# Performance work log

Measured on AMD Instinct MI355X. Metric: run time of the kernel, lower is better.

## Reference

```python
import jax, jax.numpy as jnp
import numpy as np

D_MODEL = 1024
NHEAD = 16
HEAD_DIM = D_MODEL // NHEAD
MAX_LEN = 4096
ROPE_BASE = 500.0


def _rope_tables(L, dim):
    inv_freq = 1.0 / (ROPE_BASE ** (jnp.arange(0, dim, 2, dtype=jnp.float32) / dim))
    t = jnp.arange(L, dtype=jnp.float32)
    freqs = jnp.einsum('i,j->ij', t, inv_freq)  # [L, dim/2]
    emb = jnp.concatenate([freqs, freqs], axis=-1)  # [L, dim]
    return jnp.cos(emb), jnp.sin(emb)


def _rotate_half(x):
    x1, x2 = jnp.split(x, 2, axis=-1)
    return jnp.concatenate([-x2, x1], axis=-1)


def _apply_rope(x, cos, sin):
    return x * cos + _rotate_half(x) * sin


def setup_inputs() -> dict:
    key = jax.random.key(0)
    ks = jax.random.split(key, 6)
    B, L = 4, 2048
    bound_qkv = 1.0 / np.sqrt(D_MODEL)
    x = jax.random.normal(ks[0], (B, L, D_MODEL), dtype=jnp.float32)
    key_padding_mask = jnp.zeros((B, L), dtype=bool)
    W_qkv = jax.random.uniform(ks[1], (3 * D_MODEL, D_MODEL), jnp.float32, -bound_qkv, bound_qkv)
    b_qkv = jax.random.uniform(ks[2], (3 * D_MODEL,), jnp.float32, -bound_qkv, bound_qkv)
    W_out = jax.random.uniform(ks[3], (D_MODEL, D_MODEL), jnp.float32, -bound_qkv, bound_qkv)
    b_out = jax.random.uniform(ks[4], (D_MODEL,), jnp.float32, -bound_qkv, bound_qkv)
    return {"x": x, "key_padding_mask": key_padding_mask,
            "W_qkv": W_qkv, "b_qkv": b_qkv, "W_out": W_out, "b_out": b_out}


def reference(x, key_padding_mask, W_qkv, b_qkv, W_out, b_out):
    B, L, D = x.shape
    H, hd = NHEAD, HEAD_DIM
    qkv = x @ W_qkv.T + b_qkv  # [B, L, 3D]
    q, k, v = jnp.split(qkv, 3, axis=-1)
    # [B, H, L, hd]
    q = q.reshape(B, L, H, hd).transpose(0, 2, 1, 3)
    k = k.reshape(B, L, H, hd).transpose(0, 2, 1, 3)
    v = v.reshape(B, L, H, hd).transpose(0, 2, 1, 3)
    cos, sin = _rope_tables(L, hd)  # [L, hd]
    q = _apply_rope(q, cos, sin)
    k = _apply_rope(k, cos, sin)
    scores = jnp.einsum('bhqd,bhkd->bhqk', q, k) / jnp.sqrt(jnp.float32(hd))
    mask = key_padding_mask[:, None, None, :]  # [B,1,1,L]
    scores = jnp.where(mask, -jnp.inf, scores)
    attn = jax.nn.softmax(scores, axis=-1)
    out = jnp.einsum('bhqk,bhkd->bhqd', attn, v)
    out = out.transpose(0, 2, 1, 3).reshape(B, L, D)
    return out @ W_out.T + b_out
```

## Files before the change

kernel.cpp:

```cpp
#include <hip/hip_runtime.h>
#include <stdint.h>

typedef __attribute__((ext_vector_type(8))) __bf16 bf16x8;
typedef __attribute__((ext_vector_type(4))) short short4v;
typedef __attribute__((ext_vector_type(4))) float f32x4;

#if __has_builtin(__builtin_amdgcn_exp2f)
#define EXP2(x) __builtin_amdgcn_exp2f(x)
#else
#define EXP2(x) exp2f(x)
#endif

__device__ __forceinline__ short f2bf(float f) {
  union { float f; uint32_t u; } v; v.f = f;
  uint32_t r = (v.u + 0x7fffu + ((v.u >> 16) & 1u)) >> 16;
  return (short)(uint16_t)r;
}

__device__ __forceinline__ uint32_t pk2bf(float a, float b) {
  union { __bf16 h; uint16_t u; } x, y;
  x.h = (__bf16)a; y.h = (__bf16)b;
  return (uint32_t)x.u | ((uint32_t)y.u << 16);
}

__device__ __forceinline__ void gl2lds16(const void* g, const void* lds) {
  __builtin_amdgcn_global_load_lds(
      (const __attribute__((address_space(1))) void*)(uintptr_t)g,
      (__attribute__((address_space(3))) void*)(uint32_t)(uintptr_t)lds,
      16, 0, 0);
}

__device__ __forceinline__ bf16x8 frag8(const short* p) {
  return *(const bf16x8*)(const void*)p;
}

__global__ void convert3_k(const float* __restrict__ s0, short* __restrict__ d0, int n0,
                           const float* __restrict__ s1, short* __restrict__ d1, int n1,
                           const float* __restrict__ s2, short* __restrict__ d2, int n2) {
  int i = blockIdx.x * blockDim.x + threadIdx.x;
  int t0 = n0 >> 2, t1 = t0 + (n1 >> 2), t2 = t1 + (n2 >> 2);
  const float* s; short* d; int off;
  if (i < t0) { s = s0; d = d0; off = i; }
  else if (i < t1) { s = s1; d = d1; off = i - t0; }
  else if (i < t2) { s = s2; d = d2; off = i - t1; }
  else return;
  float4 v = ((const float4*)s)[off];
  short4v o;
  o.x = f2bf(v.x); o.y = f2bf(v.y); o.z = f2bf(v.z); o.w = f2bf(v.w);
  *(short4v*)(d + off * 4) = o;
}

__global__ void rope_tab_k(float* __restrict__ cosT, float* __restrict__ sinT,
                           const unsigned char* __restrict__ mask, float* __restrict__ maskf) {
  int i = blockIdx.x * blockDim.x + threadIdx.x;
  int pos = i >> 5, j = i & 31;
  float invf = exp2f(-(float)j * (8.965784284662087f / 32.0f));
  float ang = (float)pos * invf;
  float s, c;
  sincosf(ang, &s, &c);
  cosT[i] = c; sinT[i] = s;
  if (i < 8192) maskf[i] = mask[i] ? -1e30f : 0.0f;
}

template <int EPI>
__global__ __launch_bounds__(256, 3)
void gemm_bt_k(const short* __restrict__ A, const short* __restrict__ Bm,
               const float* __restrict__ bias, int N, int K,
               float* __restrict__ Cout,
               const float* __restrict__ cosT, const float* __restrict__ sinT,
               short* __restrict__ Qb, short* __restrict__ Kb, short* __restrict__ Vt) {
  __shared__ short As[2][128 * 32];
  __shared__ short Bs[2][128 * 32];
  const int tid = threadIdx.x;
  const int lane = tid & 63;
  const int w = tid >> 6;
  const int g = lane >> 4, l15 = lane & 15;
  const int wm = (w >> 1) * 64, wn = (w & 1) * 64;
  const int bm = blockIdx.x, bn = blockIdx.y;

  const int rseg = lane >> 2;
  const int cofs = ((lane & 3) ^ ((lane >> 3) & 3)) * 8;
  const int sA0 = w, sA1 = w + 4;
  const int arow0 = (bm * 128 + sA0 * 16 + rseg) * K;
  const int arow1 = (bm * 128 + sA1 * 16 + rseg) * K;
  const int brow0 = (bn * 128 + sA0 * 16 + rseg) * K;
  const int brow1 = (bn * 128 + sA1 * 16 + rseg) * K;

  const int rsw = (l15 >> 1) & 3;

  f32x4 acc[4][4];
#pragma unroll
  for (int i = 0; i < 4; i++)
#pragma unroll
    for (int j = 0; j < 4; j++) acc[i][j] = f32x4{0.f, 0.f, 0.f, 0.f};

  gl2lds16(A + arow0 + cofs, &As[0][sA0 * 512]);
  gl2lds16(A + arow1 + cofs, &As[0][sA1 * 512]);
  gl2lds16(Bm + brow0 + cofs, &Bs[0][sA0 * 512]);
  gl2lds16(Bm + brow1 + cofs, &Bs[0][sA1 * 512]);

  int cur = 0;
  for (int k0 = 0; k0 < K; k0 += 32, cur ^= 1) {
    __syncthreads();
    int nxt = cur ^ 1;
    int k1 = k0 + 32;
    if (k1 < K) {
      gl2lds16(A + arow0 + k1 + cofs, &As[nxt][sA0 * 512]);
      gl2lds16(A + arow1 + k1 + cofs, &As[nxt][sA1 * 512]);
      gl2lds16(Bm + brow0 + k1 + cofs, &Bs[nxt][sA0 * 512]);
      gl2lds16(Bm + brow1 + k1 + cofs, &Bs[nxt][sA1 * 512]);
    }
    bf16x8 af[4], bf[4];
#pragma unroll
    for (int im = 0; im < 4; im++) af[im] = frag8(&As[cur][(wm + im * 16 + l15) * 32 + (g ^ rsw) * 8]);
#pragma unroll
    for (int jn = 0; jn < 4; jn++) bf[jn] = frag8(&Bs[cur][(wn + jn * 16 + l15) * 32 + (g ^ rsw) * 8]);
#pragma unroll
    for (int im = 0; im < 4; im++)
#pragma unroll
      for (int jn = 0; jn < 4; jn++)
        acc[im][jn] = __builtin_amdgcn_mfma_f32_16x16x32_bf16(af[im], bf[jn], acc[im][jn], 0, 0, 0);
  }

  const int row0 = bm * 128 + wm + g * 4;
  const int col0 = bn * 128 + wn;

  if (EPI == 0) {
#pragma unroll
    for (int jn = 0; jn < 4; jn++) {
      float bb = bias[col0 + jn * 16 + l15];
#pragma unroll
      for (int im = 0; im < 4; im++)
#pragma unroll
        for (int r = 0; r < 4; r++) {
          int row = row0 + im * 16 + r;
          Cout[row * N + col0 + jn * 16 + l15] = acc[im][jn][r] + bb;
        }
    }
  } else {
#pragma unroll
    for (int jn = 0; jn < 4; jn++) {
      float bb = bias[col0 + jn * 16 + l15];
#pragma unroll
      for (int im = 0; im < 4; im++)
#pragma unroll
        for (int r = 0; r < 4; r++) acc[im][jn][r] += bb;
    }
    const int sector = col0 >> 10;
    const int h = (col0 & 1023) >> 6;
    if (sector == 2) {
#pragma unroll
      for (int jn = 0; jn < 4; jn++) {
        int d = jn * 16 + l15;
#pragma unroll
        for (int im = 0; im < 4; im++) {
          int row = row0 + im * 16;
          int b = row >> 11, pos = row & 2047;
          union { uint32_t u[2]; short4v s4; } pw;
          pw.u[0] = pk2bf(acc[im][jn][0], acc[im][jn][1]);
          pw.u[1] = pk2bf(acc[im][jn][2], acc[im][jn][3]);
          *(short4v*)&Vt[((b * 16 + h) * 64 + d) * 2048 + pos] = pw.s4;
        }
      }
    } else {
      short* dst = (sector == 0) ? Qb : Kb;
      const float scl = (sector == 0) ? 0.18033688011112042f : 1.0f;
#pragma unroll
      for (int jn = 0; jn < 4; jn++) {
        int d = jn * 16 + l15;
        int j = d & 31;
#pragma unroll
        for (int im = 0; im < 4; im++)
#pragma unroll
          for (int r = 0; r < 4; r++) {
            int row = row0 + im * 16 + r;
            int b = row >> 11, pos = row & 2047;
            float c = cosT[pos * 32 + j];
            float s = sinT[pos * 32 + j];
            float xv = acc[im][jn][r];
            float xp = acc[im][jn ^ 2][r];
            float rot = (jn < 2) ? -xp : xp;
            dst[((b * 16 + h) * 2048 + pos) * 64 + d] = f2bf((xv * c + rot * s) * scl);
          }
      }
    }
  }
}

__global__ __launch_bounds__(128, 4)
void attn_k(const short* __restrict__ Qb, const short* __restrict__ Kb,
            const short* __restrict__ Vt, const float* __restrict__ maskf,
            short* __restrict__ attn) {
  __shared__ short Ks[2][32 * 64];
  __shared__ short Vs[2][64 * 32];
  __shared__ short Ps[2][32 * 32];
  const int tid = threadIdx.x, lane = tid & 63, w = tid >> 6;
  const int g = lane >> 4, l15 = lane & 15;
  const int swk = l15 & 7;
  const int fv = (l15 ^ (l15 >> 2)) & 3;
  const int qt = blockIdx.x, bh = blockIdx.y;
  const int b = bh >> 4, h = bh & 15;

  bf16x8 aq[2][2];
#pragma unroll
  for (int qi = 0; qi < 2; qi++)
#pragma unroll
    for (int kc = 0; kc < 2; kc++) {
      int q = qt * 64 + w * 32 + qi * 16 + l15;
      aq[qi][kc] = *(const bf16x8*)(const void*)(Qb + (bh * 2048 + q) * 64 + kc * 32 + g * 8);
    }
  bf16x8 aone;
#pragma unroll
  for (int i = 0; i < 8; i++) aone[i] = (__bf16)1.0f;

  f32x4 o[4][2];
#pragma unroll
  for (int jd = 0; jd < 4; jd++)
#pragma unroll
    for (int qi = 0; qi < 2; qi++) o[jd][qi] = f32x4{0.f, 0.f, 0.f, 0.f};
  f32x4 lacc[2] = {f32x4{0.f, 0.f, 0.f, 0.f}, f32x4{0.f, 0.f, 0.f, 0.f}};

  const float* mfp = maskf + b * 2048;

  const int kr8 = lane >> 3;
  const int kcst = (lane & 7) ^ kr8;
  const int vrs = lane >> 2;
  const int vcs = (lane & 3) ^ ((vrs ^ (vrs >> 2)) & 3);

  if (w == 0) {
#pragma unroll
    for (int s = 0; s < 4; s++)
      gl2lds16(Kb + (bh * 2048 + s * 8 + kr8) * 64 + kcst * 8, &Ks[0][s * 512]);
  } else {
#pragma unroll
    for (int s = 0; s < 4; s++)
      gl2lds16(Vt + (bh * 64 + s * 16 + vrs) * 2048 + vcs * 8, &Vs[0][s * 512]);
  }

  int cur = 0;
  for (int kt = 0; kt < 64; kt++, cur ^= 1) {
    const int kbase = kt * 32;
    __syncthreads();
    int nxt = cur ^ 1;
    if (kt + 1 < 64) {
      const int nb = kbase + 32;
      if (w == 0) {
#pragma unroll
        for (int s = 0; s < 4; s++)
          gl2lds16(Kb + (bh * 2048 + nb + s * 8 + kr8) * 64 + kcst * 8, &Ks[nxt][s * 512]);
      } else {
#pragma unroll
        for (int s = 0; s < 4; s++)
          gl2lds16(Vt + (bh * 64 + s * 16 + vrs) * 2048 + nb + vcs * 8, &Vs[nxt][s * 512]);
      }
    }

    f32x4 sv[2][2];
#pragma unroll
    for (int kvt = 0; kvt < 2; kvt++) {
      f32x4 mf = *(const f32x4*)(mfp + kbase + kvt * 16 + g * 4);
      sv[kvt][0] = mf; sv[kvt][1] = mf;
    }
#pragma unroll
    for (int kvt = 0; kvt < 2; kvt++)
#pragma unroll
      for (int kc = 0; kc < 2; kc++) {
        bf16x8 ak = frag8(&Ks[cur][(kvt * 16 + l15) * 64 + ((kc * 4 + g) ^ swk) * 8]);
        sv[kvt][0] = __builtin_amdgcn_mfma_f32_16x16x32_bf16(ak, aq[0][kc], sv[kvt][0], 0, 0, 0);
        sv[kvt][1] = __builtin_amdgcn_mfma_f32_16x16x32_bf16(ak, aq[1][kc], sv[kvt][1], 0, 0, 0);
      }

#pragma unroll
    for (int qi = 0; qi < 2; qi++)
#pragma unroll
      for (int kvt = 0; kvt < 2; kvt++) {
        union { uint32_t u[2]; short4v s4; } pw;
        pw.u[0] = pk2bf(EXP2(sv[kvt][qi][0]), EXP2(sv[kvt][qi][1]));
        pw.u[1] = pk2bf(EXP2(sv[kvt][qi][2]), EXP2(sv[kvt][qi][3]));
        *(short4v*)&Ps[w][(qi * 16 + l15) * 32 + (((kvt * 2 + (g >> 1)) ^ fv) * 8) + (g & 1) * 4] = pw.s4;
      }

    {
      bf16x8 av[4];
#pragma unroll
      for (int jd = 0; jd < 4; jd++)
        av[jd] = frag8(&Vs[cur][(jd * 16 + l15) * 32 + (g ^ fv) * 8]);
#pragma unroll
      for (int qi = 0; qi < 2; qi++) {
        bf16x8 bp = frag8(&Ps[w][(qi * 16 + l15) * 32 + (g ^ fv) * 8]);
#pragma unroll
        for (int jd = 0; jd < 4; jd++)
          o[jd][qi] = __builtin_amdgcn_mfma_f32_16x16x32_bf16(av[jd], bp, o[jd][qi], 0, 0, 0);
        lacc[qi] = __builtin_amdgcn_mfma_f32_16x16x32_bf16(aone, bp, lacc[qi], 0, 0, 0);
      }
    }
  }

#pragma unroll
  for (int qi = 0; qi < 2; qi++) {
    float inv = 1.0f / lacc[qi][0];
    int q = qt * 64 + w * 32 + qi * 16 + l15;
#pragma unroll
    for (int jd = 0; jd < 4; jd++) {
      union { uint32_t u[2]; short4v s4; } pw;
      pw.u[0] = pk2bf(o[jd][qi][0] * inv, o[jd][qi][1] * inv);
      pw.u[1] = pk2bf(o[jd][qi][2] * inv, o[jd][qi][3] * inv);
      *(short4v*)&attn[(b * 2048 + q) * 1024 + h * 64 + jd * 16 + g * 4] = pw.s4;
    }
  }
}

extern "C" void kernel_launch(void* const* d_in, const int* in_sizes, int n_in,
                              void* d_out, int out_size, void* d_ws, size_t ws_size,
                              hipStream_t stream) {
  const float* x = (const float*)d_in[0];
  const unsigned char* mask = (const unsigned char*)d_in[1];
  const float* W_qkv = (const float*)d_in[2];
  const float* b_qkv = (const float*)d_in[3];
  const float* W_out = (const float*)d_in[4];
  const float* b_out = (const float*)d_in[5];
  float* out = (float*)d_out;

  char* ws = (char*)d_ws;
  short* xb    = (short*)(ws + 0);
  short* wqkvb = (short*)(ws + 16777216);
  short* woutb = (short*)(ws + 23068672);
  float* cosT  = (float*)(ws + 25165824);
  float* sinT  = (float*)(ws + 25427968);
  short* Qb    = (short*)(ws + 25690112);
  short* Kb    = (short*)(ws + 42467328);
  short* Vtb   = (short*)(ws + 59244544);
  short* attnb = (short*)(ws + 76021760);
  float* maskf = (float*)(ws + 92798976);

  convert3_k<<<12288, 256, 0, stream>>>(x, xb, 8388608, W_qkv, wqkvb, 3145728, W_out, woutb, 1048576);
  rope_tab_k<<<256, 256, 0, stream>>>(cosT, sinT, mask, maskf);
  gemm_bt_k<1><<<dim3(64, 24), 256, 0, stream>>>(xb, wqkvb, b_qkv, 3072, 1024,
                                                 nullptr, cosT, sinT, Qb, Kb, Vtb);
  attn_k<<<dim3(32, 64), 128, 0, stream>>>(Qb, Kb, Vtb, maskf, attnb);
  gemm_bt_k<0><<<dim3(64, 8), 256, 0, stream>>>(attnb, woutb, b_out, 1024, 1024,
                                                out, nullptr, nullptr, nullptr, nullptr, nullptr);
}
```

Measured before the change: 293.9 us.

## Load K/V fragments directly from global into registers, one wave per 64 queries

```diff
diff --git a/kernel.cpp b/kernel.cpp
--- a/kernel.cpp
+++ b/kernel.cpp
@@ -187,119 +187,111 @@
   }
 }
 
-__global__ __launch_bounds__(128, 4)
+__global__ __launch_bounds__(64, 2)
 void attn_k(const short* __restrict__ Qb, const short* __restrict__ Kb,
             const short* __restrict__ Vt, const float* __restrict__ maskf,
             short* __restrict__ attn) {
-  __shared__ short Ks[2][32 * 64];
-  __shared__ short Vs[2][64 * 32];
-  __shared__ short Ps[2][32 * 32];
-  const int tid = threadIdx.x, lane = tid & 63, w = tid >> 6;
+  __shared__ short Ps[64 * 32];
+  const int lane = threadIdx.x & 63;
   const int g = lane >> 4, l15 = lane & 15;
-  const int swk = l15 & 7;
   const int fv = (l15 ^ (l15 >> 2)) & 3;
-  const int qt = blockIdx.x, bh = blockIdx.y;
+  const int bh = blockIdx.x, qw = blockIdx.y;
   const int b = bh >> 4, h = bh & 15;
-
-  bf16x8 aq[2][2];
-#pragma unroll
-  for (int qi = 0; qi < 2; qi++)
-#pragma unroll
-    for (int kc = 0; kc < 2; kc++) {
-      int q = qt * 64 + w * 32 + qi * 16 + l15;
-      aq[qi][kc] = *(const bf16x8*)(const void*)(Qb + (bh * 2048 + q) * 64 + kc * 32 + g * 8);
-    }
+  const int q0 = qw * 64;
+
+  bf16x8 aq[4][2];
+#pragma unroll
+  for (int qi = 0; qi < 4; qi++)
+#pragma unroll
+    for (int kc = 0; kc < 2; kc++)
+      aq[qi][kc] = frag8(Qb + (bh * 2048 + q0 + qi * 16 + l15) * 64 + kc * 32 + g * 8);
+
   bf16x8 aone;
 #pragma unroll
   for (int i = 0; i < 8; i++) aone[i] = (__bf16)1.0f;
 
-  f32x4 o[4][2];
+  f32x4 o[4][4];
 #pragma unroll
   for (int jd = 0; jd < 4; jd++)
 #pragma unroll
-    for (int qi = 0; qi < 2; qi++) o[jd][qi] = f32x4{0.f, 0.f, 0.f, 0.f};
-  f32x4 lacc[2] = {f32x4{0.f, 0.f, 0.f, 0.f}, f32x4{0.f, 0.f, 0.f, 0.f}};
-
-  const float* mfp = maskf + b * 2048;
-
-  const int kr8 = lane >> 3;
-  const int kcst = (lane & 7) ^ kr8;
-  const int vrs = lane >> 2;
-  const int vcs = (lane & 3) ^ ((vrs ^ (vrs >> 2)) & 3);
-
-  if (w == 0) {
-#pragma unroll
-    for (int s = 0; s < 4; s++)
-      gl2lds16(Kb + (bh * 2048 + s * 8 + kr8) * 64 + kcst * 8, &Ks[0][s * 512]);
-  } else {
-#pragma unroll
-    for (int s = 0; s < 4; s++)
-      gl2lds16(Vt + (bh * 64 + s * 16 + vrs) * 2048 + vcs * 8, &Vs[0][s * 512]);
-  }
-
-  int cur = 0;
-  for (int kt = 0; kt < 64; kt++, cur ^= 1) {
+    for (int qi = 0; qi < 4; qi++) o[jd][qi] = f32x4{0.f, 0.f, 0.f, 0.f};
+  f32x4 lacc[4];
+#pragma unroll
+  for (int qi = 0; qi < 4; qi++) lacc[qi] = f32x4{0.f, 0.f, 0.f, 0.f};
+
+  const short* kp = Kb + (bh * 2048 + l15) * 64 + g * 8;
+  const short* vp = Vt + (bh * 64 + l15) * 2048 + g * 8;
+  const float* mp = maskf + b * 2048 + g * 4;
+
+  bf16x8 kf[2][2], kn[2][2];
+  f32x4 mf2[2], mn2[2];
+#pragma unroll
+  for (int kvt = 0; kvt < 2; kvt++) {
+#pragma unroll
+    for (int kc = 0; kc < 2; kc++) kf[kvt][kc] = frag8(kp + (kvt * 16) * 64 + kc * 32);
+    mf2[kvt] = *(const f32x4*)(mp + kvt * 16);
+  }
+
+  for (int kt = 0; kt < 64; kt++) {
     const int kbase = kt * 32;
-    __syncthreads();
-    int nxt = cur ^ 1;
     if (kt + 1 < 64) {
       const int nb = kbase + 32;
-      if (w == 0) {
-#pragma unroll
-        for (int s = 0; s < 4; s++)
-          gl2lds16(Kb + (bh * 2048 + nb + s * 8 + kr8) * 64 + kcst * 8, &Ks[nxt][s * 512]);
-      } else {
-#pragma unroll
-        for (int s = 0; s < 4; s++)
-          gl2lds16(Vt + (bh * 64 + s * 16 + vrs) * 2048 + nb + vcs * 8, &Vs[nxt][s * 512]);
+#pragma unroll
+      for (int kvt = 0; kvt < 2; kvt++) {
+#pragma unroll
+        for (int kc = 0; kc < 2; kc++) kn[kvt][kc] = frag8(kp + (nb + kvt * 16) * 64 + kc * 32);
+        mn2[kvt] = *(const f32x4*)(mp + nb + kvt * 16);
       }
     }
-
-    f32x4 sv[2][2];
-#pragma unroll
-    for (int kvt = 0; kvt < 2; kvt++) {
-      f32x4 mf = *(const f32x4*)(mfp + kbase + kvt * 16 + g * 4);
-      sv[kvt][0] = mf; sv[kvt][1] = mf;
-    }
+    bf16x8 vf[4];
+#pragma unroll
+    for (int jd = 0; jd < 4; jd++)
+      vf[jd] = frag8(vp + (jd * 16) * 2048 + kbase);
+
+    f32x4 sv[4][2];
+#pragma unroll
+    for (int qi = 0; qi < 4; qi++)
+#pragma unroll
+      for (int kvt = 0; kvt < 2; kvt++) sv[qi][kvt] = mf2[kvt];
 #pragma unroll
     for (int kvt = 0; kvt < 2; kvt++)
 #pragma unroll
-      for (int kc = 0; kc < 2; kc++) {
-        bf16x8 ak = frag8(&Ks[cur][(kvt * 16 + l15) * 64 + ((kc * 4 + g) ^ swk) * 8]);
-        sv[kvt][0] = __builtin_amdgcn_mfma_f32_16x16x32_bf16(ak, aq[0][kc], sv[kvt][0], 0, 0, 0);
-        sv[kvt][1] = __builtin_amdgcn_mfma_f32_16x16x32_bf16(ak, aq[1][kc], sv[kvt][1], 0, 0, 0);
-      }
-
-#pragma unroll
-    for (int qi = 0; qi < 2; qi++)
+      for (int kc = 0; kc < 2; kc++)
+#pragma unroll
+        for (int qi = 0; qi < 4; qi++)
+          sv[qi][kvt] = __builtin_amdgcn_mfma_f32_16x16x32_bf16(kf[kvt][kc], aq[qi][kc], sv[qi][kvt], 0, 0, 0);
+
+#pragma unroll
+    for (int qi = 0; qi < 4; qi++)
 #pragma unroll
       for (int kvt = 0; kvt < 2; kvt++) {
         union { uint32_t u[2]; short4v s4; } pw;
-        pw.u[0] = pk2bf(EXP2(sv[kvt][qi][0]), EXP2(sv[kvt][qi][1]));
-        pw.u[1] = pk2bf(EXP2(sv[kvt][qi][2]), EXP2(sv[kvt][qi][3]));
-        *(short4v*)&Ps[w][(qi * 16 + l15) * 32 + (((kvt * 2 + (g >> 1)) ^ fv) * 8) + (g & 1) * 4] = pw.s4;
+        pw.u[0] = pk2bf(EXP2(sv[qi][kvt][0]), EXP2(sv[qi][kvt][1]));
+        pw.u[1] = pk2bf(EXP2(sv[qi][kvt][2]), EXP2(sv[qi][kvt][3]));
+        *(short4v*)&Ps[(qi * 16 + l15) * 32 + (((kvt * 2 + (g >> 1)) ^ fv) * 8) + (g & 1) * 4] = pw.s4;
       }
 
-    {
-      bf16x8 av[4];
+#pragma unroll
+    for (int qi = 0; qi < 4; qi++) {
+      bf16x8 bp = frag8(&Ps[(qi * 16 + l15) * 32 + (g ^ fv) * 8]);
 #pragma unroll
       for (int jd = 0; jd < 4; jd++)
-        av[jd] = frag8(&Vs[cur][(jd * 16 + l15) * 32 + (g ^ fv) * 8]);
-#pragma unroll
-      for (int qi = 0; qi < 2; qi++) {
-        bf16x8 bp = frag8(&Ps[w][(qi * 16 + l15) * 32 + (g ^ fv) * 8]);
-#pragma unroll
-        for (int jd = 0; jd < 4; jd++)
-          o[jd][qi] = __builtin_amdgcn_mfma_f32_16x16x32_bf16(av[jd], bp, o[jd][qi], 0, 0, 0);
-        lacc[qi] = __builtin_amdgcn_mfma_f32_16x16x32_bf16(aone, bp, lacc[qi], 0, 0, 0);
-      }
-    }
-  }
-
-#pragma unroll
-  for (int qi = 0; qi < 2; qi++) {
+        o[jd][qi] = __builtin_amdgcn_mfma_f32_16x16x32_bf16(vf[jd], bp, o[jd][qi], 0, 0, 0);
+      lacc[qi] = __builtin_amdgcn_mfma_f32_16x16x32_bf16(aone, bp, lacc[qi], 0, 0, 0);
+    }
+
+#pragma unroll
+    for (int kvt = 0; kvt < 2; kvt++) {
+#pragma unroll
+      for (int kc = 0; kc < 2; kc++) kf[kvt][kc] = kn[kvt][kc];
+      mf2[kvt] = mn2[kvt];
+    }
+  }
+
+#pragma unroll
+  for (int qi = 0; qi < 4; qi++) {
     float inv = 1.0f / lacc[qi][0];
-    int q = qt * 64 + w * 32 + qi * 16 + l15;
+    int q = q0 + qi * 16 + l15;
 #pragma unroll
     for (int jd = 0; jd < 4; jd++) {
       union { uint32_t u[2]; short4v s4; } pw;
@@ -337,7 +329,7 @@
   rope_tab_k<<<256, 256, 0, stream>>>(cosT, sinT, mask, maskf);
   gemm_bt_k<1><<<dim3(64, 24), 256, 0, stream>>>(xb, wqkvb, b_qkv, 3072, 1024,
                                                  nullptr, cosT, sinT, Qb, Kb, Vtb);
-  attn_k<<<dim3(32, 64), 128, 0, stream>>>(Qb, Kb, Vtb, maskf, attnb);
+  attn_k<<<dim3(64, 32), 64, 0, stream>>>(Qb, Kb, Vtb, maskf, attnb);
   gemm_bt_k<0><<<dim3(64, 8), 256, 0, stream>>>(attnb, woutb, b_out, 1024, 1024,
                                                 out, nullptr, nullptr, nullptr, nullptr, nullptr);
 }
```

New measurement: 321.9 us. 1.1x slower.
